# Performance work log

Measured on AMD Instinct MI355X. Metric: run time of the kernel, lower is better.

Reference implementation:

```python
import jax, jax.numpy as jnp
import numpy as np

C_EMB = 64  # n_embd


def setup_inputs() -> dict:
    key = jax.random.key(0)
    ks = jax.random.split(key, 7)
    B, T, C, H, BS = 2, 512, C_EMB, 64, 512
    s = lambda k, shp, sc: (jax.random.normal(k, shp, dtype=jnp.float32) * sc)
    return {
        "x": s(ks[0], (B, T, C), 1.0),
        "pos_table": s(ks[1], (BS, C), 0.02),
        "W1": s(ks[2], (C, 4 * C), (4 * C) ** -0.5),  # Linear(4C -> C), torch layout [out,in]
        "b1": s(ks[3], (C,), 0.01),
        "W2": s(ks[4], (1, C), C ** -0.5),            # Linear(C -> 1)
        "b2": s(ks[5], (1,), 0.01),
        "Wv": s(ks[6], (H, C), C ** -0.5),            # Linear(C -> H, bias=False)
    }


def reference(x, pos_table, W1, b1, W2, b2, Wv):
    B, T, C = x.shape
    # x1 = cat([pos_emb, x], -1): [B,T,2C]
    pos = pos_table[:T]  # [T,C]
    x1 = jnp.concatenate([jnp.broadcast_to(pos[None], (B, T, C)), x], axis=-1)  # [B,T,2C]
    # a2[b,i,j] = cat([x1[b,j], x1[b,i]]); Linear(4C->C) splits into key/query halves.
    Wk = W1[:, : 2 * C]   # acts on x1_j
    Wq = W1[:, 2 * C :]   # acts on x1_i
    hk = jnp.einsum('btd,cd->btc', x1, Wk)  # [B,T,C] indexed by j
    hq = jnp.einsum('btd,cd->btc', x1, Wq)  # [B,T,C] indexed by i
    hidden = jax.nn.relu(hq[:, :, None, :] + hk[:, None, :, :] + b1)  # [B,T(i),T(j),C]
    scores = jnp.einsum('bijc,c->bij', hidden, W2[0]) + b2[0]          # [B,T,T]
    wei = scores * (C ** -0.5)
    causal = jnp.tril(jnp.ones((T, T), dtype=bool))
    wei = jnp.where(causal[None], wei, -jnp.inf)
    wei = jax.nn.softmax(wei, axis=-1)  # dropout p=0 -> identity
    v = jnp.einsum('btc,hc->bth', x, Wv)  # [B,T,H]
    return jnp.einsum('bij,bjh->bih', wei, v)
```

## Files before the change

### kernel.cpp

```cpp
#include <hip/hip_runtime.h>
#include <math.h>

constexpr int TLEN = 512;
constexpr int CDIM = 64;
constexpr int BDIM = 2;

__global__ __launch_bounds__(256) void hk_kernel(
    const float* __restrict__ x, const float* __restrict__ pos,
    const float* __restrict__ W1, float4* __restrict__ hkt4)
{
    const int tid = threadIdx.x;
    const int r0g = blockIdx.x * 4;
    const int b   = r0g >> 9;
    const int t0  = r0g & (TLEN - 1);

    __shared__ float4 wk_s[64 * 32];
    __shared__ alignas(16) float x1s[4][128];
    __shared__ float hks[CDIM][5];

    const float4* W1f4 = (const float4*)W1;
    #pragma unroll
    for (int m = tid; m < 64 * 32; m += 256) {
        const int c = m >> 5, e4 = m & 31;
        wk_s[c * 32 + (e4 ^ (c & 31))] = W1f4[c * 64 + e4];
    }
    #pragma unroll
    for (int e = tid; e < 4 * 128; e += 256) {
        const int r4 = e >> 7, d = e & 127;
        const int grow = r0g + r4;
        const int tt = grow & (TLEN - 1);
        x1s[r4][d] = (d < CDIM) ? pos[tt * CDIM + d]
                                : x[grow * CDIM + (d - CDIM)];
    }
    __syncthreads();

    {
        const int sub = tid >> 6, c = tid & 63;
        const float4* xv = (const float4*)x1s[sub];
        const float4* wb = wk_s + c * 32;
        const int sw = c & 31;
        float4 a = make_float4(0.f, 0.f, 0.f, 0.f);
        #pragma unroll
        for (int d4 = 0; d4 < 32; ++d4) {
            const float4 xx = xv[d4];
            const float4 ww = wb[d4 ^ sw];
            a.x = fmaf(xx.x, ww.x, a.x); a.y = fmaf(xx.y, ww.y, a.y);
            a.z = fmaf(xx.z, ww.z, a.z); a.w = fmaf(xx.w, ww.w, a.w);
        }
        hks[c][sub] = (a.x + a.y) + (a.z + a.w);
    }
    __syncthreads();

    if (tid < 64) {
        const int c4 = tid >> 2, tl = tid & 3;
        const float4 v = make_float4(hks[c4 * 4 + 0][tl], hks[c4 * 4 + 1][tl],
                                     hks[c4 * 4 + 2][tl], hks[c4 * 4 + 3][tl]);
        hkt4[(b * 16 + c4) * TLEN + t0 + tl] = v;
    }
}

__global__ __launch_bounds__(512, 4) void attn_kernel(
    const float* __restrict__ x,  const float* __restrict__ pos,
    const float* __restrict__ W1, const float* __restrict__ b1,
    const float* __restrict__ W2, const float* __restrict__ b2,
    const float* __restrict__ Wv, const float4* __restrict__ hkt4,
    float* __restrict__ out)
{
    const int tid = threadIdx.x;
    const int idx = blockIdx.x;
    const int b   = idx & 1;
    const int p   = idx >> 1;
    int rr[2];
    rr[0] = p; rr[1] = (TLEN - 1) - p;

    __shared__ float4 wq_s[64 * 32];
    __shared__ float4 wv_s[64 * 16];
    __shared__ alignas(16) float x1s[2][128];
    __shared__ float hqp[2][CDIM][4];
    __shared__ alignas(16) float hq_sf[2][CDIM];
    __shared__ float4 w24_s[16];
    __shared__ alignas(16) float pS[2][TLEN];
    __shared__ float2 wreds[8];
    __shared__ float pvs[2][8][CDIM];
    __shared__ alignas(16) float o_s[2][CDIM];

    const float4* W1f4 = (const float4*)W1;
    #pragma unroll
    for (int m = tid; m < 64 * 32; m += 512) {
        const int c = m >> 5, e4 = m & 31;
        wq_s[c * 32 + (e4 ^ (c & 31))] = W1f4[c * 64 + 32 + e4];
    }
    const float4* Wvf4 = (const float4*)Wv;
    #pragma unroll
    for (int m = tid; m < 64 * 16; m += 512) {
        const int hh = m >> 4, e4 = m & 15;
        wv_s[hh * 16 + (e4 ^ (hh & 15))] = Wvf4[hh * 16 + e4];
    }
    if (tid < 256) {
        const int rp = tid >> 7, d = tid & 127;
        const int i  = rr[rp];
        x1s[rp][d] = (d < CDIM) ? pos[i * CDIM + d]
                                : x[(b * TLEN + i) * CDIM + (d - CDIM)];
    } else if (tid < 272) {
        w24_s[tid - 256] = ((const float4*)W2)[tid - 256];
    }
    __syncthreads();

    {
        const int k = tid >> 8, part = (tid >> 6) & 3, c = tid & 63;
        const float4* xv = ((const float4*)x1s[k]) + part * 8;
        const float4* wb = wq_s + c * 32;
        const int sw = c & 31;
        float4 a = make_float4(0.f, 0.f, 0.f, 0.f);
        #pragma unroll
        for (int d4 = 0; d4 < 8; ++d4) {
            const float4 xx = xv[d4];
            const float4 ww = wb[(part * 8 + d4) ^ sw];
            a.x = fmaf(xx.x, ww.x, a.x); a.y = fmaf(xx.y, ww.y, a.y);
            a.z = fmaf(xx.z, ww.z, a.z); a.w = fmaf(xx.w, ww.w, a.w);
        }
        hqp[k][c][part] = (a.x + a.y) + (a.z + a.w);
    }
    __syncthreads();
    if (tid < 128) {
        const int k = tid >> 6, c = tid & 63;
        hq_sf[k][c] = hqp[k][c][0] + hqp[k][c][1] + hqp[k][c][2]
                    + hqp[k][c][3] + b1[c];
    }
    __syncthreads();

    const float b2v = b2[0];
    const float4* hk4b = hkt4 + b * 16 * TLEN;
    const int j = tid;
    const int w = tid >> 6;

    float swv[2];
    #pragma unroll
    for (int k = 0; k < 2; ++k) {
        const int rk = rr[k];
        if ((w << 6) <= rk) {
            const float4* hq4 = (const float4*)hq_sf[k];
            float4 acc = make_float4(0.f, 0.f, 0.f, 0.f);
            #pragma unroll
            for (int c4 = 0; c4 < 16; ++c4) {
                const float4 kk = hk4b[c4 * TLEN + j];
                const float4 qq = hq4[c4];
                const float4 w2v = w24_s[c4];
                acc.x = fmaf(fmaxf(kk.x + qq.x, 0.f), w2v.x, acc.x);
                acc.y = fmaf(fmaxf(kk.y + qq.y, 0.f), w2v.y, acc.y);
                acc.z = fmaf(fmaxf(kk.z + qq.z, 0.f), w2v.z, acc.z);
                acc.w = fmaf(fmaxf(kk.w + qq.w, 0.f), w2v.w, acc.w);
            }
            const bool vld = (j <= rk);
            const float sv = ((acc.x + acc.y) + (acc.z + acc.w) + b2v) * 0.125f;
            const float pt = vld ? __expf(sv) : 0.f;
            pS[k][j] = pt;
            float sm = pt;
            #pragma unroll
            for (int off = 32; off > 0; off >>= 1)
                sm += __shfl_xor(sm, off);
            swv[k] = sm;
        } else {
            swv[k] = 0.f;
        }
    }
    if ((tid & 63) == 0) wreds[w] = make_float2(swv[0], swv[1]);
    __syncthreads();

    const int h = tid & 63;
    const int g = w;
    const float* xh = x + b * TLEN * CDIM + h;
    const int nj4 = (rr[1] >> 2) + 1;
    float4 a0 = make_float4(0.f, 0.f, 0.f, 0.f);
    float4 a1 = a0;
    for (int j4 = g; j4 < nj4; j4 += 8) {
        const int j0 = j4 * 4;
        const float4 p1v = ((const float4*)pS[1])[j4];
        const float x0 = xh[j0 * CDIM];
        const float x1 = xh[(j0 + 1) * CDIM];
        const float x2 = xh[(j0 + 2) * CDIM];
        const float x3 = xh[(j0 + 3) * CDIM];
        a1.x = fmaf(p1v.x, x0, a1.x); a1.y = fmaf(p1v.y, x1, a1.y);
        a1.z = fmaf(p1v.z, x2, a1.z); a1.w = fmaf(p1v.w, x3, a1.w);
        if (j0 <= rr[0]) {
            const float4 p0v = ((const float4*)pS[0])[j4];
            a0.x = fmaf(p0v.x, x0, a0.x); a0.y = fmaf(p0v.y, x1, a0.y);
            a0.z = fmaf(p0v.z, x2, a0.z); a0.w = fmaf(p0v.w, x3, a0.w);
        }
    }
    pvs[0][g][h] = (a0.x + a0.y) + (a0.z + a0.w);
    pvs[1][g][h] = (a1.x + a1.y) + (a1.z + a1.w);
    __syncthreads();
    if (tid < 128) {
        const int k = tid >> 6, hh = tid & 63;
        float o = pvs[k][0][hh];
        #pragma unroll
        for (int ww = 1; ww < 8; ++ww) o += pvs[k][ww][hh];
        float gsum = 0.f;
        #pragma unroll
        for (int ww = 0; ww < 8; ++ww)
            gsum += (k == 0) ? wreds[ww].x : wreds[ww].y;
        o_s[k][hh] = o / gsum;
    }
    __syncthreads();
    if (tid < 128) {
        const int k = tid >> 6, hh = tid & 63;
        const float4* wb = wv_s + hh * 16;
        const int sw = hh & 15;
        const float4* o4 = (const float4*)o_s[k];
        float4 a = make_float4(0.f, 0.f, 0.f, 0.f);
        #pragma unroll
        for (int c4 = 0; c4 < 16; ++c4) {
            const float4 wwv = wb[c4 ^ sw];
            const float4 oo = o4[c4];
            a.x = fmaf(oo.x, wwv.x, a.x); a.y = fmaf(oo.y, wwv.y, a.y);
            a.z = fmaf(oo.z, wwv.z, a.z); a.w = fmaf(oo.w, wwv.w, a.w);
        }
        out[(b * TLEN + rr[k]) * CDIM + hh] = (a.x + a.y) + (a.z + a.w);
    }
}

extern "C" void kernel_launch(void* const* d_in, const int* in_sizes, int n_in,
                              void* d_out, int out_size, void* d_ws, size_t ws_size,
                              hipStream_t stream)
{
    const float* x   = (const float*)d_in[0];
    const float* pos = (const float*)d_in[1];
    const float* W1  = (const float*)d_in[2];
    const float* b1  = (const float*)d_in[3];
    const float* W2  = (const float*)d_in[4];
    const float* b2  = (const float*)d_in[5];
    const float* Wv  = (const float*)d_in[6];
    float* out = (float*)d_out;

    float4* hkt4 = (float4*)d_ws;

    hk_kernel<<<BDIM * TLEN / 4, 256, 0, stream>>>(x, pos, W1, hkt4);
    attn_kernel<<<BDIM * TLEN / 2, 512, 0, stream>>>(x, pos, W1, b1, W2, b2, Wv,
                                                     hkt4, out);
}
```

Measured before the change: 18.73 us.

## Compute query projection in projection kernel and share key loads across both rows

Moves the hq projection (with bias) from the attention kernel into the first kernel, which now loads the full W1 and writes hk and hq to workspace. The attention kernel no longer stages Wq in shared memory or runs a per-block matvec and its extra barriers. It also fuses the two row score loops so each hk load serves both query rows. The cost is a larger shared-memory footprint in the first kernel (64 KB of W1) and extra global traffic for hq.

Result: slower. 23.09 us (+23.3%).

```diff
diff --git a/kernel.cpp b/kernel.cpp
--- a/kernel.cpp
+++ b/kernel.cpp
@@ -5,24 +5,25 @@
 constexpr int CDIM = 64;
 constexpr int BDIM = 2;
 
-__global__ __launch_bounds__(256) void hk_kernel(
+__global__ __launch_bounds__(256) void proj_kernel(
     const float* __restrict__ x, const float* __restrict__ pos,
-    const float* __restrict__ W1, float4* __restrict__ hkt4)
+    const float* __restrict__ W1, const float* __restrict__ b1,
+    float4* __restrict__ hkt4, float* __restrict__ hqb)
 {
     const int tid = threadIdx.x;
     const int r0g = blockIdx.x * 4;
     const int b   = r0g >> 9;
     const int t0  = r0g & (TLEN - 1);
 
-    __shared__ float4 wk_s[64 * 32];
+    __shared__ float4 w1_s[64 * 64];
     __shared__ alignas(16) float x1s[4][128];
     __shared__ float hks[CDIM][5];
 
     const float4* W1f4 = (const float4*)W1;
     #pragma unroll
-    for (int m = tid; m < 64 * 32; m += 256) {
-        const int c = m >> 5, e4 = m & 31;
-        wk_s[c * 32 + (e4 ^ (c & 31))] = W1f4[c * 64 + e4];
+    for (int m = tid; m < 64 * 64; m += 256) {
+        const int c = m >> 6, e4 = m & 63;
+        w1_s[c * 64 + (e4 ^ (c & 63))] = W1f4[c * 64 + e4];
     }
     #pragma unroll
     for (int e = tid; e < 4 * 128; e += 256) {
@@ -36,18 +37,24 @@
 
     {
         const int sub = tid >> 6, c = tid & 63;
+        const int grow = r0g + sub;
         const float4* xv = (const float4*)x1s[sub];
-        const float4* wb = wk_s + c * 32;
-        const int sw = c & 31;
-        float4 a = make_float4(0.f, 0.f, 0.f, 0.f);
+        const float4* wb = w1_s + c * 64;
+        const int sw = c & 63;
+        float4 ak = make_float4(0.f, 0.f, 0.f, 0.f);
+        float4 aq = ak;
         #pragma unroll
         for (int d4 = 0; d4 < 32; ++d4) {
             const float4 xx = xv[d4];
-            const float4 ww = wb[d4 ^ sw];
-            a.x = fmaf(xx.x, ww.x, a.x); a.y = fmaf(xx.y, ww.y, a.y);
-            a.z = fmaf(xx.z, ww.z, a.z); a.w = fmaf(xx.w, ww.w, a.w);
-        }
-        hks[c][sub] = (a.x + a.y) + (a.z + a.w);
+            const float4 wk = wb[d4 ^ sw];
+            const float4 wq = wb[(32 + d4) ^ sw];
+            ak.x = fmaf(xx.x, wk.x, ak.x); ak.y = fmaf(xx.y, wk.y, ak.y);
+            ak.z = fmaf(xx.z, wk.z, ak.z); ak.w = fmaf(xx.w, wk.w, ak.w);
+            aq.x = fmaf(xx.x, wq.x, aq.x); aq.y = fmaf(xx.y, wq.y, aq.y);
+            aq.z = fmaf(xx.z, wq.z, aq.z); aq.w = fmaf(xx.w, wq.w, aq.w);
+        }
+        hks[c][sub] = (ak.x + ak.y) + (ak.z + ak.w);
+        hqb[grow * CDIM + c] = (aq.x + aq.y) + (aq.z + aq.w) + b1[c];
     }
     __syncthreads();
 
@@ -60,10 +67,9 @@
 }
 
 __global__ __launch_bounds__(512, 4) void attn_kernel(
-    const float* __restrict__ x,  const float* __restrict__ pos,
-    const float* __restrict__ W1, const float* __restrict__ b1,
-    const float* __restrict__ W2, const float* __restrict__ b2,
-    const float* __restrict__ Wv, const float4* __restrict__ hkt4,
+    const float* __restrict__ x,   const float* __restrict__ W2,
+    const float* __restrict__ b2,  const float* __restrict__ Wv,
+    const float4* __restrict__ hkt4, const float4* __restrict__ hqb4,
     float* __restrict__ out)
 {
     const int tid = threadIdx.x;
@@ -73,59 +79,25 @@
     int rr[2];
     rr[0] = p; rr[1] = (TLEN - 1) - p;
 
-    __shared__ float4 wq_s[64 * 32];
     __shared__ float4 wv_s[64 * 16];
-    __shared__ alignas(16) float x1s[2][128];
-    __shared__ float hqp[2][CDIM][4];
-    __shared__ alignas(16) float hq_sf[2][CDIM];
+    __shared__ float4 hq_s[2][16];
     __shared__ float4 w24_s[16];
     __shared__ alignas(16) float pS[2][TLEN];
     __shared__ float2 wreds[8];
     __shared__ float pvs[2][8][CDIM];
     __shared__ alignas(16) float o_s[2][CDIM];
 
-    const float4* W1f4 = (const float4*)W1;
-    #pragma unroll
-    for (int m = tid; m < 64 * 32; m += 512) {
-        const int c = m >> 5, e4 = m & 31;
-        wq_s[c * 32 + (e4 ^ (c & 31))] = W1f4[c * 64 + 32 + e4];
-    }
     const float4* Wvf4 = (const float4*)Wv;
     #pragma unroll
     for (int m = tid; m < 64 * 16; m += 512) {
         const int hh = m >> 4, e4 = m & 15;
         wv_s[hh * 16 + (e4 ^ (hh & 15))] = Wvf4[hh * 16 + e4];
     }
-    if (tid < 256) {
-        const int rp = tid >> 7, d = tid & 127;
-        const int i  = rr[rp];
-        x1s[rp][d] = (d < CDIM) ? pos[i * CDIM + d]
-                                : x[(b * TLEN + i) * CDIM + (d - CDIM)];
-    } else if (tid < 272) {
-        w24_s[tid - 256] = ((const float4*)W2)[tid - 256];
-    }
-    __syncthreads();
-
-    {
-        const int k = tid >> 8, part = (tid >> 6) & 3, c = tid & 63;
-        const float4* xv = ((const float4*)x1s[k]) + part * 8;
-        const float4* wb = wq_s + c * 32;
-        const int sw = c & 31;
-        float4 a = make_float4(0.f, 0.f, 0.f, 0.f);
-        #pragma unroll
-        for (int d4 = 0; d4 < 8; ++d4) {
-            const float4 xx = xv[d4];
-            const float4 ww = wb[(part * 8 + d4) ^ sw];
-            a.x = fmaf(xx.x, ww.x, a.x); a.y = fmaf(xx.y, ww.y, a.y);
-            a.z = fmaf(xx.z, ww.z, a.z); a.w = fmaf(xx.w, ww.w, a.w);
-        }
-        hqp[k][c][part] = (a.x + a.y) + (a.z + a.w);
-    }
-    __syncthreads();
-    if (tid < 128) {
-        const int k = tid >> 6, c = tid & 63;
-        hq_sf[k][c] = hqp[k][c][0] + hqp[k][c][1] + hqp[k][c][2]
-                    + hqp[k][c][3] + b1[c];
+    if (tid < 32) {
+        const int rp = tid >> 4, e = tid & 15;
+        hq_s[rp][e] = hqb4[(b * TLEN + rr[rp]) * 16 + e];
+    } else if (tid < 48) {
+        w24_s[tid - 32] = ((const float4*)W2)[tid - 32];
     }
     __syncthreads();
 
@@ -133,38 +105,61 @@
     const float4* hk4b = hkt4 + b * 16 * TLEN;
     const int j = tid;
     const int w = tid >> 6;
-
-    float swv[2];
-    #pragma unroll
-    for (int k = 0; k < 2; ++k) {
-        const int rk = rr[k];
-        if ((w << 6) <= rk) {
-            const float4* hq4 = (const float4*)hq_sf[k];
-            float4 acc = make_float4(0.f, 0.f, 0.f, 0.f);
-            #pragma unroll
-            for (int c4 = 0; c4 < 16; ++c4) {
-                const float4 kk = hk4b[c4 * TLEN + j];
-                const float4 qq = hq4[c4];
-                const float4 w2v = w24_s[c4];
-                acc.x = fmaf(fmaxf(kk.x + qq.x, 0.f), w2v.x, acc.x);
-                acc.y = fmaf(fmaxf(kk.y + qq.y, 0.f), w2v.y, acc.y);
-                acc.z = fmaf(fmaxf(kk.z + qq.z, 0.f), w2v.z, acc.z);
-                acc.w = fmaf(fmaxf(kk.w + qq.w, 0.f), w2v.w, acc.w);
-            }
-            const bool vld = (j <= rk);
-            const float sv = ((acc.x + acc.y) + (acc.z + acc.w) + b2v) * 0.125f;
-            const float pt = vld ? __expf(sv) : 0.f;
-            pS[k][j] = pt;
-            float sm = pt;
-            #pragma unroll
-            for (int off = 32; off > 0; off >>= 1)
-                sm += __shfl_xor(sm, off);
-            swv[k] = sm;
-        } else {
-            swv[k] = 0.f;
-        }
-    }
-    if ((tid & 63) == 0) wreds[w] = make_float2(swv[0], swv[1]);
+    const bool act0 = ((w << 6) <= rr[0]);
+
+    float4 acc0 = make_float4(0.f, 0.f, 0.f, 0.f);
+    float4 acc1 = acc0;
+    if (act0) {
+        #pragma unroll
+        for (int c4 = 0; c4 < 16; ++c4) {
+            const float4 kk = hk4b[c4 * TLEN + j];
+            const float4 q0 = hq_s[0][c4];
+            const float4 q1 = hq_s[1][c4];
+            const float4 ww = w24_s[c4];
+            acc0.x = fmaf(fmaxf(kk.x + q0.x, 0.f), ww.x, acc0.x);
+            acc0.y = fmaf(fmaxf(kk.y + q0.y, 0.f), ww.y, acc0.y);
+            acc0.z = fmaf(fmaxf(kk.z + q0.z, 0.f), ww.z, acc0.z);
+            acc0.w = fmaf(fmaxf(kk.w + q0.w, 0.f), ww.w, acc0.w);
+            acc1.x = fmaf(fmaxf(kk.x + q1.x, 0.f), ww.x, acc1.x);
+            acc1.y = fmaf(fmaxf(kk.y + q1.y, 0.f), ww.y, acc1.y);
+            acc1.z = fmaf(fmaxf(kk.z + q1.z, 0.f), ww.z, acc1.z);
+            acc1.w = fmaf(fmaxf(kk.w + q1.w, 0.f), ww.w, acc1.w);
+        }
+    } else {
+        #pragma unroll
+        for (int c4 = 0; c4 < 16; ++c4) {
+            const float4 kk = hk4b[c4 * TLEN + j];
+            const float4 q1 = hq_s[1][c4];
+            const float4 ww = w24_s[c4];
+            acc1.x = fmaf(fmaxf(kk.x + q1.x, 0.f), ww.x, acc1.x);
+            acc1.y = fmaf(fmaxf(kk.y + q1.y, 0.f), ww.y, acc1.y);
+            acc1.z = fmaf(fmaxf(kk.z + q1.z, 0.f), ww.z, acc1.z);
+            acc1.w = fmaf(fmaxf(kk.w + q1.w, 0.f), ww.w, acc1.w);
+        }
+    }
+
+    float sw0 = 0.f, sw1;
+    if (act0) {
+        const float sv = ((acc0.x + acc0.y) + (acc0.z + acc0.w) + b2v) * 0.125f;
+        const float pt = (j <= rr[0]) ? __expf(sv) : 0.f;
+        pS[0][j] = pt;
+        float sm = pt;
+        #pragma unroll
+        for (int off = 32; off > 0; off >>= 1)
+            sm += __shfl_xor(sm, off);
+        sw0 = sm;
+    }
+    {
+        const float sv = ((acc1.x + acc1.y) + (acc1.z + acc1.w) + b2v) * 0.125f;
+        const float pt = (j <= rr[1]) ? __expf(sv) : 0.f;
+        pS[1][j] = pt;
+        float sm = pt;
+        #pragma unroll
+        for (int off = 32; off > 0; off >>= 1)
+            sm += __shfl_xor(sm, off);
+        sw1 = sm;
+    }
+    if ((tid & 63) == 0) wreds[w] = make_float2(sw0, sw1);
     __syncthreads();
 
     const int h = tid & 63;
@@ -234,8 +229,10 @@
     float* out = (float*)d_out;
 
     float4* hkt4 = (float4*)d_ws;
-
-    hk_kernel<<<BDIM * TLEN / 4, 256, 0, stream>>>(x, pos, W1, hkt4);
-    attn_kernel<<<BDIM * TLEN / 2, 512, 0, stream>>>(x, pos, W1, b1, W2, b2, Wv,
-                                                     hkt4, out);
+    float*  hqb  = (float*)d_ws + 4 * 16384;
+
+    proj_kernel<<<BDIM * TLEN / 4, 256, 0, stream>>>(x, pos, W1, b1, hkt4, hqb);
+    attn_kernel<<<BDIM * TLEN / 2, 512, 0, stream>>>(x, W2, b2, Wv,
+                                                     hkt4, (const float4*)hqb,
+                                                     out);
 }
```

## Pack both causal rows' score work into one pass over threads

Applied to the files above, without the earlier changes.

Each block handles rows p and 511-p, whose valid columns add up to 513. Instead of two masked passes over all 512 threads, each thread now computes exactly one score for row 1 or row 0, and the last thread computes the one leftover element. The change is meant to remove the wasted masked lanes and the second sequential score loop. In exchange it adds extra zero padding writes for the float4 PV reads and leaves thread 511 with a serial extra workload.

Measured after the change: 19.07 us. No clear change (+1.8%).

```diff
diff --git a/kernel.cpp b/kernel.cpp
--- a/kernel.cpp
+++ b/kernel.cpp
@@ -133,38 +133,62 @@
     const float4* hk4b = hkt4 + b * 16 * TLEN;
     const int j = tid;
     const int w = tid >> 6;
-
-    float swv[2];
-    #pragma unroll
-    for (int k = 0; k < 2; ++k) {
-        const int rk = rr[k];
-        if ((w << 6) <= rk) {
-            const float4* hq4 = (const float4*)hq_sf[k];
-            float4 acc = make_float4(0.f, 0.f, 0.f, 0.f);
-            #pragma unroll
-            for (int c4 = 0; c4 < 16; ++c4) {
-                const float4 kk = hk4b[c4 * TLEN + j];
-                const float4 qq = hq4[c4];
-                const float4 w2v = w24_s[c4];
-                acc.x = fmaf(fmaxf(kk.x + qq.x, 0.f), w2v.x, acc.x);
-                acc.y = fmaf(fmaxf(kk.y + qq.y, 0.f), w2v.y, acc.y);
-                acc.z = fmaf(fmaxf(kk.z + qq.z, 0.f), w2v.z, acc.z);
-                acc.w = fmaf(fmaxf(kk.w + qq.w, 0.f), w2v.w, acc.w);
-            }
-            const bool vld = (j <= rk);
-            const float sv = ((acc.x + acc.y) + (acc.z + acc.w) + b2v) * 0.125f;
-            const float pt = vld ? __expf(sv) : 0.f;
-            pS[k][j] = pt;
-            float sm = pt;
-            #pragma unroll
-            for (int off = 32; off > 0; off >>= 1)
-                sm += __shfl_xor(sm, off);
-            swv[k] = sm;
-        } else {
-            swv[k] = 0.f;
-        }
-    }
-    if ((tid & 63) == 0) wreds[w] = make_float2(swv[0], swv[1]);
+    const int n1 = TLEN - p;
+    const bool isR1 = (j < n1);
+    const int myrow = isR1 ? 1 : 0;
+    const int mycol = isR1 ? j : j - n1;
+
+    float pt;
+    {
+        const float4* hq4 = (const float4*)hq_sf[myrow];
+        float4 acc = make_float4(0.f, 0.f, 0.f, 0.f);
+        #pragma unroll
+        for (int c4 = 0; c4 < 16; ++c4) {
+            const float4 kk = hk4b[c4 * TLEN + mycol];
+            const float4 qq = hq4[c4];
+            const float4 ww = w24_s[c4];
+            acc.x = fmaf(fmaxf(kk.x + qq.x, 0.f), ww.x, acc.x);
+            acc.y = fmaf(fmaxf(kk.y + qq.y, 0.f), ww.y, acc.y);
+            acc.z = fmaf(fmaxf(kk.z + qq.z, 0.f), ww.z, acc.z);
+            acc.w = fmaf(fmaxf(kk.w + qq.w, 0.f), ww.w, acc.w);
+        }
+        const float sv = ((acc.x + acc.y) + (acc.z + acc.w) + b2v) * 0.125f;
+        pt = __expf(sv);
+    }
+    pS[myrow][mycol] = pt;
+
+    float ptx = 0.f;
+    if (j == TLEN - 1) {
+        const float4* hq4 = (const float4*)hq_sf[0];
+        float4 acc = make_float4(0.f, 0.f, 0.f, 0.f);
+        #pragma unroll
+        for (int c4 = 0; c4 < 16; ++c4) {
+            const float4 kk = hk4b[c4 * TLEN + p];
+            const float4 qq = hq4[c4];
+            const float4 ww = w24_s[c4];
+            acc.x = fmaf(fmaxf(kk.x + qq.x, 0.f), ww.x, acc.x);
+            acc.y = fmaf(fmaxf(kk.y + qq.y, 0.f), ww.y, acc.y);
+            acc.z = fmaf(fmaxf(kk.z + qq.z, 0.f), ww.z, acc.z);
+            acc.w = fmaf(fmaxf(kk.w + qq.w, 0.f), ww.w, acc.w);
+        }
+        const float sv = ((acc.x + acc.y) + (acc.z + acc.w) + b2v) * 0.125f;
+        ptx = __expf(sv);
+        pS[0][p] = ptx;
+    }
+    if (j < 3) {
+        if (p + 1 + j < TLEN)     pS[0][p + 1 + j] = 0.f;
+        if (rr[1] + 1 + j < TLEN) pS[1][rr[1] + 1 + j] = 0.f;
+    }
+
+    float c0 = isR1 ? 0.f : pt;
+    float c1 = isR1 ? pt : 0.f;
+    c0 += ptx;
+    #pragma unroll
+    for (int off = 32; off > 0; off >>= 1) {
+        c0 += __shfl_xor(c0, off);
+        c1 += __shfl_xor(c1, off);
+    }
+    if ((tid & 63) == 0) wreds[w] = make_float2(c0, c1);
     __syncthreads();
 
     const int h = tid & 63;
```
